# Optimization experiments

Measured on AMD Instinct MI355X. Metric: run time of the kernel, lower is better.

Reference implementation:

```python
import jax, jax.numpy as jnp
import numpy as np

N_G, E_G = 50000, 800000
N_S, E_S = 10000, 160000
NF = 64
B = 8

def _w(key, shape):
    fan_in = shape[-1]
    return jax.random.normal(key, shape, dtype=jnp.float32) / np.sqrt(fan_in)

def setup_inputs() -> dict:
    key = jax.random.key(0)
    ks = jax.random.split(key, 40)
    inp = {
        "graph_x": jax.random.normal(ks[0], (N_G, NF), dtype=jnp.float32),
        "subgraph_x": jax.random.normal(ks[1], (N_S, NF), dtype=jnp.float32),
        "point": jax.random.normal(ks[2], (B, NF), dtype=jnp.float32),
        "graph_edge_index": jax.random.randint(ks[3], (2, E_G), 0, N_G),
        "graph_batch": jnp.sort(jax.random.randint(ks[4], (N_G,), 0, B)),
        "subgraph_edge_index": jax.random.randint(ks[5], (2, E_S), 0, N_S),
        "subgraph_batch": jnp.sort(jax.random.randint(ks[6], (N_S,), 0, B)),
    }
    # GraphConv params per branch: channel sizes 64->128->256->192
    dims = [(2 * NF, NF), (4 * NF, 2 * NF), (3 * NF, 4 * NF)]
    i = 7
    for pre in ("g", "s"):
        for li, (o, c) in enumerate(dims, start=1):
            inp[f"{pre}W{li}r"] = _w(ks[i], (o, c)); i += 1  # lin_rel (aggregated)
            inp[f"{pre}W{li}n"] = _w(ks[i], (o, c)); i += 1  # lin_root (self)
            inp[f"{pre}B{li}"] = jnp.zeros((o,), dtype=jnp.float32)
    inp["l1W"] = _w(ks[i], (600, 3 * NF + 3 * NF + NF)); i += 1
    inp["l1b"] = jnp.zeros((600,), dtype=jnp.float32)
    inp["l2W"] = _w(ks[i], (256, 600)); i += 1
    inp["l2b"] = jnp.zeros((256,), dtype=jnp.float32)
    inp["l3W"] = _w(ks[i], (NF, 256)); i += 1
    inp["l3b"] = jnp.zeros((NF,), dtype=jnp.float32)
    return inp

def _graph_conv(x, src, dst, Wr, Wn, b, n_nodes):
    # PyG GraphConv: out_i = Wr @ sum_{j->i} x_j + Wn @ x_i + b
    agg = jax.ops.segment_sum(x[src], dst, num_segments=n_nodes)
    return agg @ Wr.T + x @ Wn.T + b

def _scatter_mean(x, seg, num_segments):
    s = jax.ops.segment_sum(x, seg, num_segments=num_segments)
    cnt = jax.ops.segment_sum(jnp.ones((x.shape[0],), x.dtype), seg, num_segments=num_segments)
    return s / jnp.maximum(cnt, 1.0)[:, None]

def _branch(x, edge_index, batch, params, n_nodes):
    src, dst = edge_index[0], edge_index[1]
    for (Wr, Wn, b) in params:
        x = jax.nn.elu(_graph_conv(x, src, dst, Wr, Wn, b, n_nodes))
    return _scatter_mean(x, batch, B)

def reference(graph_x, subgraph_x, point,
              gW1r, gW1n, gB1, gW2r, gW2n, gB2, gW3r, gW3n, gB3,
              sW1r, sW1n, sB1, sW2r, sW2n, sB2, sW3r, sW3n, sB3,
              l1W, l1b, l2W, l2b, l3W, l3b,
              graph_edge_index, graph_batch, subgraph_edge_index, subgraph_batch):
    x1 = _branch(graph_x, graph_edge_index, graph_batch,
                 [(gW1r, gW1n, gB1), (gW2r, gW2n, gB2), (gW3r, gW3n, gB3)], N_G)
    x2 = _branch(subgraph_x, subgraph_edge_index, subgraph_batch,
                 [(sW1r, sW1n, sB1), (sW2r, sW2n, sB2), (sW3r, sW3n, sB3)], N_S)
    x = jnp.concatenate([x1, x2, point], axis=-1)  # [B, 448]
    x = jax.nn.relu(x @ l1W.T + l1b)
    x = jax.nn.relu(x @ l2W.T + l2b)
    return x @ l3W.T + l3b  # [B, 64]
```

## Files before the change

kernel.cpp:

```cpp
#include <hip/hip_runtime.h>
#include <cmath>

typedef __attribute__((ext_vector_type(8))) short short8;
typedef __attribute__((ext_vector_type(4))) float floatx4;
typedef __attribute__((ext_vector_type(2))) float floatx2;
typedef __attribute__((ext_vector_type(4))) int intx4;
typedef __attribute__((ext_vector_type(2))) int intx2;

#define N_G 50000
#define E_G 800000
#define N_S 10000
#define E_S 160000
#define NT (N_G + N_S)
#define ET (E_G + E_S)
#define BATCH 8
#define STRIDE 64
#define FPASS 2
#define NTILE_T (NT / 16)
#define PSPLIT 4

__device__ __forceinline__ short f2b(float f) {
    unsigned u = __builtin_bit_cast(unsigned, f);
    u += 0x7FFF + ((u >> 16) & 1);
    return (short)(u >> 16);
}
__device__ __forceinline__ short8 fp8x8_to_bf16(intx2 w) {
    floatx2 f0 = __builtin_amdgcn_cvt_pk_f32_fp8(w[0], false);
    floatx2 f1 = __builtin_amdgcn_cvt_pk_f32_fp8(w[0], true);
    floatx2 f2 = __builtin_amdgcn_cvt_pk_f32_fp8(w[1], false);
    floatx2 f3 = __builtin_amdgcn_cvt_pk_f32_fp8(w[1], true);
    short8 r;
    r[0]=f2b(f0[0]); r[1]=f2b(f0[1]); r[2]=f2b(f1[0]); r[3]=f2b(f1[1]);
    r[4]=f2b(f2[0]); r[5]=f2b(f2[1]); r[6]=f2b(f3[0]); r[7]=f2b(f3[1]);
    return r;
}
__device__ __forceinline__ void acc16(float* acc, intx4 w) {
    #pragma unroll
    for (int q = 0; q < 4; ++q) {
        floatx2 f0 = __builtin_amdgcn_cvt_pk_f32_fp8(w[q], false);
        floatx2 f1 = __builtin_amdgcn_cvt_pk_f32_fp8(w[q], true);
        acc[q * 4 + 0] += f0[0];
        acc[q * 4 + 1] += f0[1];
        acc[q * 4 + 2] += f1[0];
        acc[q * 4 + 3] += f1[1];
    }
}
__device__ __forceinline__ void gload_lds16(const void* g, void* l) {
    __builtin_amdgcn_global_load_lds(
        (const __attribute__((address_space(1))) unsigned int*)g,
        (__attribute__((address_space(3))) unsigned int*)l, 16, 0, 0);
}

struct RepArgs { const float* Wr[6]; const float* Wn[6]; short* dst[6]; int cin[6]; int nk[6]; int groups[6]; };
__global__ void init_kernel(const float* __restrict__ gx, const float* __restrict__ sx,
                            unsigned char* __restrict__ X0_8,
                            unsigned char* __restrict__ h1_8, unsigned char* __restrict__ h2_8,
                            int* __restrict__ dcount, float* __restrict__ pooled,
                            const int* __restrict__ g_batch, const int* __restrict__ s_batch,
                            int* __restrict__ starts, int* __restrict__ csr,
                            RepArgs ra, int total_groups) {
    int t = blockIdx.x * blockDim.x + threadIdx.x;
    if (t < NT * 16) {
        size_t e = (size_t)t * 4;
        const float* src = (e < (size_t)N_G * 64) ? (gx + e) : (sx + (e - (size_t)N_G * 64));
        floatx4 v = *(const floatx4*)src;
        int w8 = 0;
        w8 = __builtin_amdgcn_cvt_pk_fp8_f32(v[0], v[1], w8, false);
        w8 = __builtin_amdgcn_cvt_pk_fp8_f32(v[2], v[3], w8, true);
        *(unsigned int*)(X0_8 + e) = (unsigned int)w8;
        intx4 s4 = {NT, NT, NT, NT};
        *(intx4*)(csr + (size_t)t * 4) = s4;
    }
    if (t < NT) dcount[t] = 0;
    if (t < 16 * 192) pooled[t] = 0.f;
    if (t < 28) {
        intx4 z = {0, 0, 0, 0};
        if (t < 4)       *(intx4*)(X0_8 + (size_t)NT * 64  + t * 16) = z;
        else if (t < 12) *(intx4*)(h1_8 + (size_t)NT * 128 + (t - 4) * 16) = z;
        else             *(intx4*)(h2_8 + (size_t)NT * 256 + (t - 12) * 16) = z;
    }
    if (t <= 16) {
        int b = t;
        if (b == 16) { starts[16] = NT; }
        else {
            int key, n, base;
            const int* arr;
            if (b < 8) { arr = g_batch; n = N_G; key = b; base = 0; }
            else       { arr = s_batch; n = N_S; key = b - 8; base = N_G; }
            int lo = 0, hi = n;
            while (lo < hi) { int mid = (lo + hi) >> 1; if (arr[mid] < key) lo = mid + 1; else hi = mid; }
            starts[b] = base + lo;
        }
    }
    if (t < total_groups) {
        int seg = 0, off = t;
        while (seg < 5 && off >= ra.groups[seg]) { off -= ra.groups[seg]; ++seg; }
        int CIN = ra.cin[seg], NK = ra.nk[seg];
        int lane = off & 63;
        int rest = off >> 6;
        int tt = rest % NK;
        int ot = rest / NK;
        int o = ot * 16 + (lane & 15);
        int kk = tt * 32 + (lane >> 4) * 8;
        const float* src = (kk < CIN) ? (ra.Wr[seg] + (size_t)o * CIN + kk)
                                      : (ra.Wn[seg] + (size_t)o * CIN + (kk - CIN));
        floatx4 u0 = *(const floatx4*)src;
        floatx4 u1 = *(const floatx4*)(src + 4);
        short8 d;
        d[0]=f2b(u0[0]); d[1]=f2b(u0[1]); d[2]=f2b(u0[2]); d[3]=f2b(u0[3]);
        d[4]=f2b(u1[0]); d[5]=f2b(u1[1]); d[6]=f2b(u1[2]); d[7]=f2b(u1[3]);
        *(short8*)(ra.dst[seg] + (size_t)off * 8) = d;
    }
}

__global__ void fill_kernel(const int* __restrict__ g_ei, const int* __restrict__ s_ei,
                            int* __restrict__ dcount, int* __restrict__ csr) {
    int pass = blockIdx.x & (FPASS - 1);
    int lb   = blockIdx.x >> 1;
    int t = lb * blockDim.x + threadIdx.x;
    if (t >= ET) return;
    int dst;
    if (t < E_G) dst = g_ei[E_G + t];
    else         dst = s_ei[E_S + (t - E_G)] + N_G;
    int lo = pass * (NT / FPASS);
    int hi = lo + (NT / FPASS);
    if (dst < lo || dst >= hi) return;
    int src;
    if (t < E_G) src = g_ei[t];
    else         src = s_ei[t - E_G] + N_G;
    int slot = atomicAdd(&dcount[dst], 1);
    if (slot < STRIDE) csr[(size_t)dst * STRIDE + slot] = src;
}

template<int C>
__global__ __launch_bounds__(256) void agg8_kernel(const unsigned char* __restrict__ x8,
                            const int* __restrict__ dcount,
                            const int* __restrict__ csr, short* __restrict__ out) {
    constexpr int C16 = C / 16;
    int t = blockIdx.x * blockDim.x + threadIdx.x;
    if (t >= NT * C16) return;
    int node = t / C16;
    int ch   = t % C16;
    const int* crow = csr + (size_t)node * STRIDE;
    int deg8 = (min(dcount[node], STRIDE) + 7) & ~7;
    const unsigned char* xb = x8 + (size_t)ch * 16;
    float acc[16];
    #pragma unroll
    for (int j = 0; j < 16; ++j) acc[j] = 0.f;
    for (int e = 0; e < deg8; e += 8) {
        intx4 i0 = *(const intx4*)(crow + e);
        intx4 i1 = *(const intx4*)(crow + e + 4);
        intx4 w0 = *(const intx4*)(xb + (size_t)i0[0] * C);
        intx4 w1 = *(const intx4*)(xb + (size_t)i0[1] * C);
        intx4 w2 = *(const intx4*)(xb + (size_t)i0[2] * C);
        intx4 w3 = *(const intx4*)(xb + (size_t)i0[3] * C);
        intx4 w4 = *(const intx4*)(xb + (size_t)i1[0] * C);
        intx4 w5 = *(const intx4*)(xb + (size_t)i1[1] * C);
        intx4 w6 = *(const intx4*)(xb + (size_t)i1[2] * C);
        intx4 w7 = *(const intx4*)(xb + (size_t)i1[3] * C);
        acc16(acc, w0); acc16(acc, w1); acc16(acc, w2); acc16(acc, w3);
        acc16(acc, w4); acc16(acc, w5); acc16(acc, w6); acc16(acc, w7);
    }
    short8 o0, o1;
    #pragma unroll
    for (int j = 0; j < 8; ++j) { o0[j] = f2b(acc[j]); o1[j] = f2b(acc[8 + j]); }
    short8* q = (short8*)(out + (size_t)node * C + ch * 16);
    q[0] = o0; q[1] = o1;
}

template<int CIN, int COUT, bool POOL>
__global__ __launch_bounds__(256) void gemm_elu_kernel(
        const short* __restrict__ A1, const unsigned char* __restrict__ A2_8,
        const short* __restrict__ gWF, const short* __restrict__ sWF,
        const float* __restrict__ gB, const float* __restrict__ sB,
        unsigned char* __restrict__ out8,
        float* __restrict__ pooled, float* __restrict__ part,
        const int* __restrict__ starts) {
    constexpr int NK  = CIN / 16;
    constexpr int NOT = COUT / 16;
    constexpr int TILE_SH = NK * 512;
    constexpr int CHUNK_SH = 8192;
    constexpr int CHUNK_OT = CHUNK_SH / TILE_SH;
    static_assert(NOT % CHUNK_OT == 0, "chunk must divide NOT");
    constexpr int NC = NOT / CHUNK_OT;
    constexpr int SREG = CHUNK_SH / 2048;
    __shared__ short lds[2][CHUNK_SH];

    int wave = threadIdx.x >> 6;
    int lane = threadIdx.x & 63;
    int tile0 = blockIdx.x << 2;
    int myTile = tile0 + wave;
    bool active = myTile < NTILE_T;
    int tileC = active ? myTile : (NTILE_T - 1);
    int r0 = tileC * 16;
    bool sub = (r0 >= N_G);
    const short* WF = sub ? sWF : gWF;
    const float* bias = sub ? sB : gB;
    int id = lane & 15, quad = lane >> 4;
    int arow = r0 + id;
    short8 a[NK];
    #pragma unroll
    for (int t = 0; t < NK; ++t) {
        int kk = t * 32 + quad * 8;
        if (kk < CIN) {
            a[t] = *(const short8*)(A1 + (size_t)arow * CIN + kk);
        } else {
            intx2 w = *(const intx2*)(A2_8 + (size_t)arow * CIN + (kk - CIN));
            a[t] = fp8x8_to_bf16(w);
        }
    }
    int seg0 = 0, seg1 = 0;
    if (POOL) {
        while (seg0 < 15 && starts[seg0 + 1] <= r0) ++seg0;
        seg1 = seg0;
        while (seg1 < 15 && starts[seg1 + 1] <= r0 + 15) ++seg1;
    }

    constexpr int BTILE = N_G / 16;
    int lastTile = min(tile0 + 3, NTILE_T - 1);
    bool mixed = (tile0 < BTILE) && (lastTile >= BTILE);

    auto epilogue = [&](int ot, floatx4 acc) {
        int o = ot * 16 + id;
        float bv = bias[o];
        float vr[4];
        #pragma unroll
        for (int r = 0; r < 4; ++r) {
            float v = acc[r] + bv;
            vr[r] = (v > 0.f) ? v : (__expf(v) - 1.f);
        }
        if (!active) return;
        if (!POOL) {
            #pragma unroll
            for (int r = 0; r < 4; ++r) {
                int nrow = r0 + quad * 4 + r;
                int w8 = __builtin_amdgcn_cvt_pk_fp8_f32(vr[r], vr[r], 0, false);
                out8[(size_t)nrow * COUT + o] = (unsigned char)(w8 & 0xFF);
            }
        } else if (seg0 == seg1) {
            float vsum = vr[0] + vr[1] + vr[2] + vr[3];
            vsum += __shfl_down(vsum, 32, 64);
            vsum += __shfl_down(vsum, 16, 64);
            if (lane < 16) part[(size_t)tileC * 192 + o] = vsum;
        } else {
            #pragma unroll
            for (int r = 0; r < 4; ++r) {
                int nrow = r0 + quad * 4 + r;
                int sg = seg0;
                while (sg < seg1 && starts[sg + 1] <= nrow) ++sg;
                atomicAdd(&pooled[sg * 192 + o], vr[r]);
            }
        }
    };

    if (!mixed) {
        auto stage = [&](int c, int buf) {
            const short* src = WF + (size_t)c * CHUNK_SH + threadIdx.x * 8;
            short* dst = &lds[buf][threadIdx.x * 8];
            #pragma unroll
            for (int i = 0; i < SREG; ++i)
                gload_lds16(src + i * 2048, dst + i * 2048);
        };
        stage(0, 0);
        __syncthreads();
        for (int c = 0; c < NC; ++c) {
            if (c + 1 < NC) stage(c + 1, (c + 1) & 1);
            const short* base = &lds[c & 1][lane * 8];
            #pragma unroll
            for (int otl = 0; otl < CHUNK_OT; ++otl) {
                floatx4 acc = {0.f, 0.f, 0.f, 0.f};
                #pragma unroll
                for (int t = 0; t < NK; ++t) {
                    short8 b = *(const short8*)(base + otl * TILE_SH + t * 512);
                    acc = __builtin_amdgcn_mfma_f32_16x16x32_bf16(a[t], b, acc, 0, 0, 0);
                }
                epilogue(c * CHUNK_OT + otl, acc);
            }
            __syncthreads();
        }
    } else {
        for (int ot = 0; ot < NOT; ++ot) {
            floatx4 acc = {0.f, 0.f, 0.f, 0.f};
            const short* wp = WF + (((size_t)ot * NK) * 64 + lane) * 8;
            #pragma unroll
            for (int t = 0; t < NK; ++t) {
                short8 b = *(const short8*)(wp + (size_t)t * 64 * 8);
                acc = __builtin_amdgcn_mfma_f32_16x16x32_bf16(a[t], b, acc, 0, 0, 0);
            }
            epilogue(ot, acc);
        }
    }
}

__global__ __launch_bounds__(256) void pool_reduce_kernel(
        const float* __restrict__ part, const int* __restrict__ starts,
        float* __restrict__ pooled) {
    int w = (blockIdx.x * blockDim.x + threadIdx.x) >> 6;
    int lane = threadIdx.x & 63;
    if (w >= 16 * 12 * PSPLIT) return;
    int sp = w % PSPLIT;
    int rest = w / PSPLIT;
    int og = rest % 12;
    int seg = rest / 12;
    int t0 = (starts[seg] + 15) >> 4;
    int t1 = starts[seg + 1] >> 4;
    int tl = lane >> 4;
    int o = og * 16 + (lane & 15);
    float acc = 0.f;
    for (int t = t0 + sp * 4 + tl; t < t1; t += PSPLIT * 4)
        acc += part[(size_t)t * 192 + o];
    acc += __shfl_down(acc, 32, 64);
    acc += __shfl_down(acc, 16, 64);
    if (lane < 16) atomicAdd(&pooled[seg * 192 + o], acc);
}

__global__ __launch_bounds__(256) void mlp1_kernel(
        const float* __restrict__ pooled, const int* __restrict__ starts,
        const float* __restrict__ point, const float* __restrict__ W,
        const float* __restrict__ bias, float* __restrict__ out) {
    int wave = (blockIdx.x * blockDim.x + threadIdx.x) >> 6;
    int lane = threadIdx.x & 63;
    if (wave >= BATCH * 600) return;
    int b = wave / 600, o = wave % 600;
    float invg = 1.f / (float)max(starts[b + 1] - starts[b], 1);
    float invs = 1.f / (float)max(starts[9 + b] - starts[8 + b], 1);
    const float* w = W + (size_t)o * 448;
    float acc = 0.f;
    for (int i = lane; i < 448; i += 64) {
        float x;
        if (i < 192)      x = pooled[b * 192 + i] * invg;
        else if (i < 384) x = pooled[(8 + b) * 192 + (i - 192)] * invs;
        else              x = point[b * 64 + (i - 384)];
        acc += x * w[i];
    }
    #pragma unroll
    for (int off = 32; off > 0; off >>= 1) acc += __shfl_down(acc, off, 64);
    if (lane == 0) out[wave] = fmaxf(acc + bias[o], 0.f);
}

__global__ __launch_bounds__(256) void dense_wave_kernel(
        const float* __restrict__ in, const float* __restrict__ W,
        const float* __restrict__ bias, float* __restrict__ out,
        int I, int O, int relu) {
    int wave = (blockIdx.x * blockDim.x + threadIdx.x) >> 6;
    int lane = threadIdx.x & 63;
    if (wave >= BATCH * O) return;
    int b = wave / O, o = wave % O;
    const float* x = in + (size_t)b * I;
    const float* w = W + (size_t)o * I;
    float acc = 0.f;
    for (int i = lane; i < I; i += 64) acc += x[i] * w[i];
    #pragma unroll
    for (int off = 32; off > 0; off >>= 1) acc += __shfl_down(acc, off, 64);
    if (lane == 0) {
        acc += bias[o];
        if (relu) acc = fmaxf(acc, 0.f);
        out[wave] = acc;
    }
}

extern "C" void kernel_launch(void* const* d_in, const int* in_sizes, int n_in,
                              void* d_out, int out_size, void* d_ws, size_t ws_size,
                              hipStream_t stream) {
    const float* graph_x = (const float*)d_in[0];
    const float* sub_x   = (const float*)d_in[1];
    const float* point   = (const float*)d_in[2];
    const int*   g_ei    = (const int*)d_in[3];
    const int*   g_batch = (const int*)d_in[4];
    const int*   s_ei    = (const int*)d_in[5];
    const int*   s_batch = (const int*)d_in[6];
    const float* gB1=(const float*)d_in[9],  *gB2=(const float*)d_in[12], *gB3=(const float*)d_in[15];
    const float* sB1=(const float*)d_in[18], *sB2=(const float*)d_in[21], *sB3=(const float*)d_in[24];
    const float* l1W=(const float*)d_in[25], *l1b=(const float*)d_in[26];
    const float* l2W=(const float*)d_in[27], *l2b=(const float*)d_in[28];
    const float* l3W=(const float*)d_in[29], *l3b=(const float*)d_in[30];

    char* ws = (char*)d_ws;
    size_t off = 0;
    auto alloc = [&](size_t bytes) -> char* {
        char* p = ws + off;
        off = (off + bytes + 255) & ~(size_t)255;
        return p;
    };
    int* dcount = (int*)alloc((size_t)NT * 4);
    int* csr = (int*)alloc((size_t)NT * STRIDE * 4);

    const int fsz[3] = {128 * 2 * 64, 256 * 2 * 128, 192 * 2 * 256};
    short* wfrag = (short*)alloc((size_t)(fsz[0] + fsz[1] + fsz[2]) * 2 * 2);
    short* gWF[3], *sWF[3];
    { size_t o2 = 0;
      for (int l = 0; l < 3; ++l) { gWF[l] = wfrag + o2; o2 += fsz[l]; }
      for (int l = 0; l < 3; ++l) { sWF[l] = wfrag + o2; o2 += fsz[l]; } }

    unsigned char* X0_8 = (unsigned char*)alloc((size_t)(NT + 1) * 64);
    short* agg = (short*)alloc((size_t)NT * 256 * 2);
    unsigned char* h1_8 = (unsigned char*)alloc((size_t)(NT + 1) * 128);
    unsigned char* h2_8 = (unsigned char*)alloc((size_t)(NT + 1) * 256);

    float* pooled = (float*)alloc(16 * 192 * 4);
    float* part = (float*)alloc((size_t)NTILE_T * 192 * 4);
    int* starts = (int*)alloc(17 * 4);
    float* mlp_h1 = (float*)alloc(BATCH * 600 * 4);
    float* mlp_h2 = (float*)alloc(BATCH * 256 * 4);

    RepArgs ra;
    const int cin_l[3] = {64, 128, 256};
    const int nk_l[3]  = {4, 8, 16};
    const int not_l[3] = {8, 16, 12};
    const int wr_idx[6] = {7, 10, 13, 16, 19, 22};
    int total_groups = 0;
    for (int s = 0; s < 6; ++s) {
        int l = s % 3;
        ra.Wr[s] = (const float*)d_in[wr_idx[s]];
        ra.Wn[s] = (const float*)d_in[wr_idx[s] + 1];
        ra.dst[s] = (s < 3) ? gWF[l] : sWF[l];
        ra.cin[s] = cin_l[l];
        ra.nk[s] = nk_l[l];
        ra.groups[s] = not_l[l] * nk_l[l] * 64;
        total_groups += ra.groups[s];
    }

    init_kernel<<<(NT * 16 + 255) / 256, 256, 0, stream>>>(graph_x, sub_x, X0_8, h1_8, h2_8,
                                                           dcount, pooled, g_batch, s_batch,
                                                           starts, csr, ra, total_groups);

    fill_kernel<<<((ET + 255) / 256) * FPASS, 256, 0, stream>>>(g_ei, s_ei, dcount, csr);

    constexpr int NW = NT / 16;
    const int gemm_blocks = (NW + 3) / 4;

    agg8_kernel<64><<<(NT * 4 + 255) / 256, 256, 0, stream>>>(X0_8, dcount, csr, agg);
    gemm_elu_kernel<64, 128, false><<<gemm_blocks, 256, 0, stream>>>(
        agg, X0_8, gWF[0], sWF[0], gB1, sB1, h1_8, nullptr, nullptr, nullptr);
    agg8_kernel<128><<<(NT * 8 + 255) / 256, 256, 0, stream>>>(h1_8, dcount, csr, agg);
    gemm_elu_kernel<128, 256, false><<<gemm_blocks, 256, 0, stream>>>(
        agg, h1_8, gWF[1], sWF[1], gB2, sB2, h2_8, nullptr, nullptr, nullptr);
    agg8_kernel<256><<<(NT * 16 + 255) / 256, 256, 0, stream>>>(h2_8, dcount, csr, agg);
    gemm_elu_kernel<256, 192, true><<<gemm_blocks, 256, 0, stream>>>(
        agg, h2_8, gWF[2], sWF[2], gB3, sB3, nullptr, pooled, part, starts);

    pool_reduce_kernel<<<(16 * 12 * PSPLIT * 64 + 255) / 256, 256, 0, stream>>>(part, starts, pooled);
    mlp1_kernel<<<(BATCH * 600 + 3) / 4, 256, 0, stream>>>(pooled, starts, point, l1W, l1b, mlp_h1);
    dense_wave_kernel<<<(BATCH * 256 + 3) / 4, 256, 0, stream>>>(mlp_h1, l2W, l2b, mlp_h2, 600, 256, 1);
    dense_wave_kernel<<<(BATCH * 64 + 3) / 4, 256, 0, stream>>>(mlp_h2, l3W, l3b, (float*)d_out, 256, 64, 0);
}
```

Baseline: 351.5 us.

## Bucket edges by destination octant before CSR fill to localize atomics

Edges are binned into eight destination-range buckets inside the init kernel, using LDS counters and one global atomic per block per bucket. The CSR fill kernel then handles each bucket with interleaved blocks, replacing the two-pass filter that read every edge twice. This should concentrate the dcount atomics and csr writes on a narrower node range at a time, improving cache locality, and halves the redundant edge reads. The cost is an extra bucket buffer, an extra tiny zero kernel, and indirect edge-index reads. Buckets are capped at a fixed capacity, so a skewed destination distribution could overflow and silently drop edges.

```diff
diff --git a/kernel.cpp b/kernel.cpp
--- a/kernel.cpp
+++ b/kernel.cpp
@@ -15,9 +15,12 @@
 #define ET (E_G + E_S)
 #define BATCH 8
 #define STRIDE 64
-#define FPASS 2
 #define NTILE_T (NT / 16)
 #define PSPLIT 4
+#define NOCT 8
+#define OCTW (NT / NOCT)
+#define BCAP 131072
+#define JMAX 533
 
 __device__ __forceinline__ short f2b(float f) {
     unsigned u = __builtin_bit_cast(unsigned, f);
@@ -51,6 +54,10 @@
         (__attribute__((address_space(3))) unsigned int*)l, 16, 0, 0);
 }
 
+__global__ void zero_kernel(int* __restrict__ bcount) {
+    if (threadIdx.x < NOCT) bcount[threadIdx.x] = 0;
+}
+
 struct RepArgs { const float* Wr[6]; const float* Wn[6]; short* dst[6]; int cin[6]; int nk[6]; int groups[6]; };
 __global__ void init_kernel(const float* __restrict__ gx, const float* __restrict__ sx,
                             unsigned char* __restrict__ X0_8,
@@ -58,8 +65,28 @@
                             int* __restrict__ dcount, float* __restrict__ pooled,
                             const int* __restrict__ g_batch, const int* __restrict__ s_batch,
                             int* __restrict__ starts, int* __restrict__ csr,
+                            const int* __restrict__ g_ei, const int* __restrict__ s_ei,
+                            int* __restrict__ bcount, int* __restrict__ bucket,
                             RepArgs ra, int total_groups) {
+    __shared__ int lcnt[NOCT], lbase[NOCT], loff[NOCT];
     int t = blockIdx.x * blockDim.x + threadIdx.x;
+
+    if (threadIdx.x < NOCT) { lcnt[threadIdx.x] = 0; loff[threadIdx.x] = 0; }
+    __syncthreads();
+    int eb = -1;
+    if (t < ET) {
+        int dst = (t < E_G) ? g_ei[E_G + t] : s_ei[E_S + (t - E_G)] + N_G;
+        eb = dst / OCTW;
+        atomicAdd(&lcnt[eb], 1);
+    }
+    __syncthreads();
+    if (threadIdx.x < NOCT) lbase[threadIdx.x] = atomicAdd(&bcount[threadIdx.x], lcnt[threadIdx.x]);
+    __syncthreads();
+    if (t < ET) {
+        int idx = lbase[eb] + atomicAdd(&loff[eb], 1);
+        if (idx < BCAP) bucket[(size_t)eb * BCAP + idx] = t;
+    }
+
     if (t < NT * 16) {
         size_t e = (size_t)t * 4;
         const float* src = (e < (size_t)N_G * 64) ? (gx + e) : (sx + (e - (size_t)N_G * 64));
@@ -114,20 +141,18 @@
 }
 
 __global__ void fill_kernel(const int* __restrict__ g_ei, const int* __restrict__ s_ei,
+                            const int* __restrict__ bcount, const int* __restrict__ bucket,
                             int* __restrict__ dcount, int* __restrict__ csr) {
-    int pass = blockIdx.x & (FPASS - 1);
-    int lb   = blockIdx.x >> 1;
-    int t = lb * blockDim.x + threadIdx.x;
-    if (t >= ET) return;
-    int dst;
-    if (t < E_G) dst = g_ei[E_G + t];
-    else         dst = s_ei[E_S + (t - E_G)] + N_G;
-    int lo = pass * (NT / FPASS);
-    int hi = lo + (NT / FPASS);
-    if (dst < lo || dst >= hi) return;
-    int src;
-    if (t < E_G) src = g_ei[t];
-    else         src = s_ei[t - E_G] + N_G;
+    int o = blockIdx.x & (NOCT - 1);
+    int j = blockIdx.x >> 3;
+    int i = j * blockDim.x + threadIdx.x;
+    int n = min(bcount[o], BCAP);
+    if (i >= n) return;
+    int e = bucket[(size_t)o * BCAP + i];
+    int dst, src;
+    if (e < E_G) { dst = g_ei[E_G + e];              src = g_ei[e]; }
+    else         { int es = e - E_G;
+                   dst = s_ei[E_S + es] + N_G;       src = s_ei[es] + N_G; }
     int slot = atomicAdd(&dcount[dst], 1);
     if (slot < STRIDE) csr[(size_t)dst * STRIDE + slot] = src;
 }
@@ -384,6 +409,8 @@
     };
     int* dcount = (int*)alloc((size_t)NT * 4);
     int* csr = (int*)alloc((size_t)NT * STRIDE * 4);
+    int* bcount = (int*)alloc(NOCT * 4);
+    int* bucket = (int*)alloc((size_t)NOCT * BCAP * 4);
 
     const int fsz[3] = {128 * 2 * 64, 256 * 2 * 128, 192 * 2 * 256};
     short* wfrag = (short*)alloc((size_t)(fsz[0] + fsz[1] + fsz[2]) * 2 * 2);
@@ -420,11 +447,14 @@
         total_groups += ra.groups[s];
     }
 
+    zero_kernel<<<1, 64, 0, stream>>>(bcount);
+
     init_kernel<<<(NT * 16 + 255) / 256, 256, 0, stream>>>(graph_x, sub_x, X0_8, h1_8, h2_8,
                                                            dcount, pooled, g_batch, s_batch,
-                                                           starts, csr, ra, total_groups);
-
-    fill_kernel<<<((ET + 255) / 256) * FPASS, 256, 0, stream>>>(g_ei, s_ei, dcount, csr);
+                                                           starts, csr, g_ei, s_ei,
+                                                           bcount, bucket, ra, total_groups);
+
+    fill_kernel<<<JMAX * NOCT, 256, 0, stream>>>(g_ei, s_ei, bcount, bucket, dcount, csr);
 
     constexpr int NW = NT / 16;
     const int gemm_blocks = (NW + 3) / 4;
```

Measured after the change: 383.6 us. +9.1%, slower.
